# Optimization experiments

Hardware: AMD Instinct MI355X
Metric: run time of the kernel (lower is better)

Reference implementation:

```python
import jax, jax.numpy as jnp
import numpy as np

N_EMBD = 1024
N_HEAD = 16
HEAD_DIM = N_EMBD // N_HEAD

def setup_inputs() -> dict:
    key = jax.random.key(0)
    ks = jax.random.split(key, 5)
    B, T, C = 2, 2048, N_EMBD
    s = 1.0 / np.sqrt(C)
    x = jax.random.normal(ks[0], (B, T, C), dtype=jnp.float32)
    W_qkv = jax.random.normal(ks[1], (C, 3 * C), dtype=jnp.float32) * s
    b_qkv = jax.random.normal(ks[2], (3 * C,), dtype=jnp.float32) * 0.02
    W_o = jax.random.normal(ks[3], (C, C), dtype=jnp.float32) * s
    b_o = jax.random.normal(ks[4], (C,), dtype=jnp.float32) * 0.02
    return {"x": x, "W_qkv": W_qkv, "b_qkv": b_qkv, "W_o": W_o, "b_o": b_o}

def reference(x, W_qkv, b_qkv, W_o, b_o):
    B, T, C = x.shape
    H, D = N_HEAD, HEAD_DIM
    scale = 1.0 / np.sqrt(D)
    qkv = jnp.einsum('btc,cf->btf', x, W_qkv) + b_qkv  # [B,T,3C]
    q, k, v = jnp.split(qkv, 3, axis=-1)
    # [B,H,T,D]
    q = q.reshape(B, T, H, D).transpose(0, 2, 1, 3)
    k = k.reshape(B, T, H, D).transpose(0, 2, 1, 3)
    v = v.reshape(B, T, H, D).transpose(0, 2, 1, 3)
    att = jnp.einsum('bhqd,bhkd->bhqk', q, k) * scale  # [B,H,T,T]
    causal = jnp.tril(jnp.ones((T, T), dtype=bool))
    att = jnp.where(causal[None, None], att, -jnp.inf)
    att = jax.nn.softmax(att, axis=-1)
    y = jnp.einsum('bhqk,bhkd->bhqd', att, v)  # [B,H,T,D]
    y = y.transpose(0, 2, 1, 3).reshape(B, T, C)
    return jnp.einsum('btc,cf->btf', y, W_o) + b_o
```

## Files before the change

### kernel.cpp

```cpp
#include <hip/hip_runtime.h>
#include <hip/hip_bf16.h>

#define TT 2048
#define BB 2
#define CC 1024
#define NH 16
#define HD 64

typedef __attribute__((ext_vector_type(8))) short short8;
typedef __attribute__((ext_vector_type(4))) short short4b;
typedef __attribute__((ext_vector_type(4))) float f32x4;

typedef unsigned int __attribute__((address_space(1))) ui_gas;
typedef unsigned int __attribute__((address_space(3))) ui_las;

#if __has_builtin(__builtin_amdgcn_mfma_f32_16x16x16bf16_1k)
#define PV16 1
#else
#define PV16 0
#endif

__device__ __forceinline__ float us2f(unsigned short u) {
    union { unsigned int i; float f; } v; v.i = ((unsigned int)u) << 16; return v.f;
}
__device__ __forceinline__ unsigned short f2us(float f) {
    union { float f; unsigned int i; } v; v.f = f;
    unsigned int i = v.i;
    unsigned int lsb = (i >> 16) & 1u;
    i += 0x7fffu + lsb;
    return (unsigned short)(i >> 16);
}
__device__ __forceinline__ unsigned int pack2_trunc(float a, float b) {
    union { float f; unsigned int u; } x, y; x.f = a; y.f = b;
    return (y.u & 0xffff0000u) | (x.u >> 16);
}

__device__ __forceinline__ void gl_lds16(const unsigned short* g, unsigned short* l) {
    __builtin_amdgcn_global_load_lds((const ui_gas*)g, (ui_las*)l, 16, 0, 0);
}

__global__ __launch_bounds__(64) void detect_kernel(
    const void* p0, const void* p1, const void* p2, const void* p3, const void* p4,
    int* flags)
{
    const void* ps[5] = {p0, p1, p2, p3, p4};
    const int lane = threadIdx.x;
    for (int k = 0; k < 5; ++k) {
        const unsigned short* u = (const unsigned short*)ps[k];
        int bad = 0;
        #pragma unroll
        for (int j = 0; j < 4; ++j) {
            float v = us2f(u[lane * 4 + j]);
            if (!(fabsf(v) < 1e4f)) bad = 1;
        }
        unsigned long long m = __ballot(bad != 0);
        if (lane == 0) flags[k] = (__popcll(m) < 4) ? 1 : 0;
    }
}

__device__ __forceinline__ float4 load4(const void* p, size_t i, int isbf) {
    if (isbf) {
        ushort4 u = *reinterpret_cast<const ushort4*>((const unsigned short*)p + i);
        return make_float4(us2f(u.x), us2f(u.y), us2f(u.z), us2f(u.w));
    } else {
        return *reinterpret_cast<const float4*>((const float*)p + i);
    }
}
__device__ __forceinline__ float load1(const void* p, size_t i, int isbf) {
    return isbf ? us2f(((const unsigned short*)p)[i]) : ((const float*)p)[i];
}

__global__ __launch_bounds__(256) void prep_kernel(
    const void* __restrict__ x, const void* __restrict__ Wqkv, const void* __restrict__ Wo,
    unsigned short* __restrict__ xb, unsigned short* __restrict__ Wqkvt,
    unsigned short* __restrict__ Wot)
{
    __shared__ float Ls[64 * 65];
    __shared__ int sh_isbf;
    const int t = threadIdx.x;
    const int bid = blockIdx.x;

    const void* src;
    int mode, sub;
    if (bid < 2048)      { mode = 0; sub = bid;        src = x; }
    else if (bid < 2816) { mode = 1; sub = bid - 2048; src = Wqkv; }
    else                 { mode = 2; sub = bid - 2816; src = Wo; }

    if (t < 64) {
        const unsigned short* u = (const unsigned short*)src;
        int bad = 0;
        #pragma unroll
        for (int j = 0; j < 4; ++j) {
            float v = us2f(u[t * 4 + j]);
            if (!(fabsf(v) < 1e4f)) bad = 1;
        }
        unsigned long long m = __ballot(bad != 0);
        if (t == 0) sh_isbf = (__popcll(m) < 4) ? 1 : 0;
    }
    __syncthreads();
    const int isbf = sh_isbf;

    if (mode == 0) {
        const size_t i = ((size_t)sub * 256 + t) * 8;
        float4 a = load4(src, i, isbf);
        float4 b = load4(src, i + 4, isbf);
        alignas(16) unsigned short pk[8];
        pk[0] = f2us(a.x); pk[1] = f2us(a.y); pk[2] = f2us(a.z); pk[3] = f2us(a.w);
        pk[4] = f2us(b.x); pk[5] = f2us(b.y); pk[6] = f2us(b.z); pk[7] = f2us(b.w);
        *reinterpret_cast<uint4*>(xb + i) = *reinterpret_cast<const uint4*>(pk);
        return;
    }

    int N, Krows, n0, k0;
    unsigned short* dst;
    if (mode == 1) { N = 3 * CC; Krows = CC; dst = Wqkvt; n0 = (sub % 48) * 64; k0 = (sub / 48) * 64; }
    else           { N = CC;     Krows = CC; dst = Wot;   n0 = (sub % 16) * 64; k0 = (sub / 16) * 64; }
    {
        const int r = t >> 2, cq = (t & 3) << 4;
        #pragma unroll
        for (int i = 0; i < 4; ++i) {
            float4 v = load4(src, (size_t)(k0 + r) * N + n0 + cq + i * 4, isbf);
            Ls[r * 65 + cq + i * 4 + 0] = v.x;
            Ls[r * 65 + cq + i * 4 + 1] = v.y;
            Ls[r * 65 + cq + i * 4 + 2] = v.z;
            Ls[r * 65 + cq + i * 4 + 3] = v.w;
        }
    }
    __syncthreads();
    {
        const int c = t & 63, kg = (t >> 6) * 16;
        alignas(16) unsigned short pk[16];
        #pragma unroll
        for (int i = 0; i < 16; ++i) pk[i] = f2us(Ls[(kg + i) * 65 + c]);
        unsigned short* d = dst + (size_t)(n0 + c) * Krows + k0 + kg;
        *reinterpret_cast<uint4*>(d + 0) = *reinterpret_cast<const uint4*>(&pk[0]);
        *reinterpret_cast<uint4*>(d + 8) = *reinterpret_cast<const uint4*>(&pk[8]);
    }
}

template<int WM, int WN, int NWM, int NWN>
__global__ __launch_bounds__(256) void gemm_mfma(
    const unsigned short* __restrict__ A,
    const unsigned short* __restrict__ Bt,
    const void* __restrict__ bias, void* __restrict__ C,
    int M, int N, int K,
    const int* __restrict__ flags, int biasfi, int cfi)
{
    constexpr int BM = WM * 16 * NWM, BN = WN * 16 * NWN;
    constexpr int ASL = BM / 16, BSL = BN / 16;

    const int bias_bf = (biasfi >= 0) ? flags[biasfi] : 0;
    const int c_bf    = (cfi >= 0) ? flags[cfi] : ((cfi == -2) ? 1 : 0);

    __shared__ __align__(16) unsigned short Asl[ASL * 512];
    __shared__ __align__(16) unsigned short Bsl[BSL * 512];

    const int tid = threadIdx.x;
    const int l  = tid & 63;
    const int w  = tid >> 6;
    const int wm = w / NWN, wn = w % NWN;
    const int bm = blockIdx.y * BM, bn = blockIdx.x * BN;
    const int lm = l & 15;
    const int lk = (l >> 4) * 8;

    f32x4 acc[WM][WN];
    #pragma unroll
    for (int i = 0; i < WM; ++i)
        #pragma unroll
        for (int j = 0; j < WN; ++j) acc[i][j] = (f32x4){0.f, 0.f, 0.f, 0.f};

    for (int k0 = 0; k0 < K; k0 += 32) {
        #pragma unroll
        for (int s = 0; s < ASL / 4; ++s) {
            const int r = w * (ASL / 4) + s;
            gl_lds16(A + (size_t)(bm + r * 16 + lm) * K + k0 + lk, &Asl[r * 512]);
        }
        #pragma unroll
        for (int s = 0; s < BSL / 4; ++s) {
            const int r = w * (BSL / 4) + s;
            gl_lds16(Bt + (size_t)(bn + r * 16 + lm) * K + k0 + lk, &Bsl[r * 512]);
        }
        __syncthreads();
        short8 af[WM], bf[WN];
        #pragma unroll
        for (int i = 0; i < WM; ++i)
            af[i] = *reinterpret_cast<const short8*>(&Asl[(WM * wm + i) * 512 + l * 8]);
        #pragma unroll
        for (int j = 0; j < WN; ++j)
            bf[j] = *reinterpret_cast<const short8*>(&Bsl[(WN * wn + j) * 512 + l * 8]);
        #pragma unroll
        for (int i = 0; i < WM; ++i)
            #pragma unroll
            for (int j = 0; j < WN; ++j)
                acc[i][j] = __builtin_amdgcn_mfma_f32_16x16x32_bf16(af[i], bf[j], acc[i][j], 0, 0, 0);
        __syncthreads();
    }

    const int quad = l >> 4;
    float bv[WN];
    #pragma unroll
    for (int j = 0; j < WN; ++j) bv[j] = load1(bias, bn + (WN * wn + j) * 16 + lm, bias_bf);

    #pragma unroll
    for (int i = 0; i < WM; ++i) {
        #pragma unroll
        for (int r = 0; r < 4; ++r) {
            const int row = bm + (WM * wm + i) * 16 + quad * 4 + r;
            #pragma unroll
            for (int j = 0; j < WN; ++j) {
                const int col = bn + (WN * wn + j) * 16 + lm;
                const float val = acc[i][j][r] + bv[j];
                if (c_bf) ((unsigned short*)C)[(size_t)row * N + col] = f2us(val);
                else      ((float*)C)[(size_t)row * N + col] = val;
            }
        }
    }
}

__global__ __launch_bounds__(256) void transpose_v(
    const unsigned short* __restrict__ qkv, unsigned short* __restrict__ Vt)
{
    __shared__ __align__(16) unsigned short Ls[64 * 72];
    const int tid = threadIdx.x;
    const int tt = blockIdx.x;
    const int bh = blockIdx.y;
    const int b = bh >> 4, h = bh & 15;
    {
        const int tok = tid & 63, w = tid >> 6;
        const unsigned short* src = qkv + (size_t)(b * TT + tt * 64 + tok) * 3 * CC + 2 * CC + h * HD;
        #pragma unroll
        for (int c2 = 0; c2 < 2; ++c2) {
            int c = 2 * w + c2;
            uint4 d = *(const uint4*)(src + c * 8);
            *(uint4*)(&Ls[tok * 72 + c * 8]) = d;
        }
    }
    __syncthreads();
    {
        const int d = tid >> 2, kq = tid & 3;
        unsigned short out[16];
        #pragma unroll
        for (int i = 0; i < 16; ++i) out[i] = Ls[(kq * 16 + i) * 72 + d];
        unsigned short* dst = Vt + (size_t)bh * HD * TT + (size_t)d * TT + tt * 64 + kq * 16;
        *(uint4*)(dst + 0) = *(uint4*)(&out[0]);
        *(uint4*)(dst + 8) = *(uint4*)(&out[8]);
    }
}

__global__ __launch_bounds__(256) void attn_mfma(
    const unsigned short* __restrict__ qkv,
    const unsigned short* __restrict__ Vt,
    unsigned short* __restrict__ y)
{
    __shared__ __align__(16) unsigned short Ksh[8 * 512];
    __shared__ __align__(16) unsigned short Vsh[1039 * 8];

    const int tid = threadIdx.x;
    const int l   = tid & 63;
    const int w   = tid >> 6;
    const int quad = l >> 4;
    const int col  = l & 15;

    const int n  = blockIdx.x;
    const int g  = n >> 3;
    const int bh = (n & 7) * 4 + (g & 3);
    const int i  = g >> 2;
    const int tA = i, tB = 31 - i;
    const int b  = bh >> 4, h = bh & 15;

    for (int s = tid; s < 1039; s += 256)
        *(uint2*)(&Vsh[s * 8 + 4]) = make_uint2(0u, 0u);

    const float QSCALE = 0.18033688f;
    short8 qfA[2], qfB[2];
    #pragma unroll
    for (int t2 = 0; t2 < 2; ++t2) {
        const int qt = t2 ? tB : tA;
        short8* qf = t2 ? qfB : qfA;
        const int token = qt * 64 + w * 16 + col;
        const unsigned short* qrow = qkv + (size_t)(b * TT + token) * 3 * CC + h * HD;
        #pragma unroll
        for (int ks = 0; ks < 2; ++ks) {
            ushort4 u0 = *(const ushort4*)(qrow + ks * 32 + quad * 8);
            ushort4 u1 = *(const ushort4*)(qrow + ks * 32 + quad * 8 + 4);
            alignas(16) unsigned short pk[8];
            pk[0] = f2us(us2f(u0.x) * QSCALE);
            pk[1] = f2us(us2f(u0.y) * QSCALE);
            pk[2] = f2us(us2f(u0.z) * QSCALE);
            pk[3] = f2us(us2f(u0.w) * QSCALE);
            pk[4] = f2us(us2f(u1.x) * QSCALE);
            pk[5] = f2us(us2f(u1.y) * QSCALE);
            pk[6] = f2us(us2f(u1.z) * QSCALE);
            pk[7] = f2us(us2f(u1.w) * QSCALE);
            qf[ks] = *(const short8*)pk;
        }
    }

    f32x4 oA[4], oB[4];
    #pragma unroll
    for (int nb = 0; nb < 4; ++nb) {
        oA[nb] = (f32x4){0.f, 0.f, 0.f, 0.f};
        oB[nb] = (f32x4){0.f, 0.f, 0.f, 0.f};
    }
    float mA = -3e38f, lAc = 0.f, mB = -3e38f, lBc = 0.f;

    const unsigned short* kbase = qkv + (size_t)b * TT * 3 * CC + CC + h * HD;
    const unsigned short* vbase = Vt + (size_t)bh * HD * TT;

    const int vd = tid >> 2, vg0 = (tid & 3) * 4;

    uint4 rk[2], rv[2];
    auto issue_loads = [&](int kt) {
        const unsigned short* ksrc = kbase + (size_t)(kt * 64 + l) * 3 * CC;
        #pragma unroll
        for (int c2 = 0; c2 < 2; ++c2) {
            const int c = 2 * w + c2;
            rk[c2] = *(const uint4*)(ksrc + c * 8);
        }
        const unsigned short* vsrc = vbase + (size_t)vd * TT + kt * 64 + vg0 * 4;
        rv[0] = *(const uint4*)(vsrc + 0);
        rv[1] = *(const uint4*)(vsrc + 8);
    };
    auto write_lds = [&]() {
        #pragma unroll
        for (int c2 = 0; c2 < 2; ++c2) {
            const int c = 2 * w + c2;
            const int ks = c >> 2, q = c & 3;
            const int slot = ((quad * 2 + ks) * 64 + q * 16 + col) * 8;
            *(uint4*)(&Ksh[slot]) = rk[c2];
        }
        *(uint2*)(&Vsh[((vg0 + 0) * 65 + vd) * 8]) = make_uint2(rv[0].x, rv[0].y);
        *(uint2*)(&Vsh[((vg0 + 1) * 65 + vd) * 8]) = make_uint2(rv[0].z, rv[0].w);
        *(uint2*)(&Vsh[((vg0 + 2) * 65 + vd) * 8]) = make_uint2(rv[1].x, rv[1].y);
        *(uint2*)(&Vsh[((vg0 + 3) * 65 + vd) * 8]) = make_uint2(rv[1].z, rv[1].w);
    };

    auto step = [&](const short8* qf, f32x4* o, float& m_i, float& l_i, bool diag) {
        f32x4 st[4];
        #pragma unroll
        for (int nb = 0; nb < 4; ++nb) {
            f32x4 acc = {0.f, 0.f, 0.f, 0.f};
            #pragma unroll
            for (int ks = 0; ks < 2; ++ks) {
                short8 kf = *(const short8*)(&Ksh[((nb * 2 + ks) * 64 + l) * 8]);
                acc = __builtin_amdgcn_mfma_f32_16x16x32_bf16(kf, qf[ks], acc, 0, 0, 0);
            }
            st[nb] = acc;
        }
        float sv[4][4];
        #pragma unroll
        for (int nb = 0; nb < 4; ++nb)
            #pragma unroll
            for (int r = 0; r < 4; ++r) {
                float v = st[nb][r];
                if (diag && (nb * 16 + quad * 4 + r > w * 16 + col)) v = -3e38f;
                sv[nb][r] = v;
            }
        float rm = sv[0][0];
        #pragma unroll
        for (int nb = 0; nb < 4; ++nb)
            #pragma unroll
            for (int r = 0; r < 4; ++r) rm = fmaxf(rm, sv[nb][r]);
        rm = fmaxf(rm, __shfl_xor(rm, 16));
        rm = fmaxf(rm, __shfl_xor(rm, 32));
        const float mn = fmaxf(m_i, rm);
        float pv[4][4];
        float rs = 0.f;
        #pragma unroll
        for (int nb = 0; nb < 4; ++nb)
            #pragma unroll
            for (int r = 0; r < 4; ++r) {
                float p = __builtin_exp2f(sv[nb][r] - mn);
                pv[nb][r] = p;
                rs += p;
            }
        rs += __shfl_xor(rs, 16);
        rs += __shfl_xor(rs, 32);
        if (__ballot(mn > m_i) != 0ull) {
            const float al = __builtin_exp2f(m_i - mn);
            l_i = l_i * al + rs;
            float alr[4];
            #pragma unroll
            for (int r = 0; r < 4; ++r) alr[r] = __shfl(al, quad * 4 + r);
            #pragma unroll
            for (int nb = 0; nb < 4; ++nb)
                #pragma unroll
                for (int r = 0; r < 4; ++r) o[nb][r] *= alr[r];
        } else {
            l_i += rs;
        }
        m_i = mn;
#if PV16
        short4b pf[4];
        #pragma unroll
        for (int nbk = 0; nbk < 4; ++nbk) {
            union { short4b s; unsigned int u[2]; } pk;
            pk.u[0] = pack2_trunc(pv[nbk][0], pv[nbk][1]);
            pk.u[1] = pack2_trunc(pv[nbk][2], pv[nbk][3]);
            pf[nbk] = pk.s;
        }
        #pragma unroll
        for (int nbd = 0; nbd < 4; ++nbd)
            #pragma unroll
            for (int nbk = 0; nbk < 4; ++nbk) {
                short4b vf = *(const short4b*)(&Vsh[((nbk * 4 + quad) * 65 + nbd * 16 + col) * 8]);
                o[nbd] = __builtin_amdgcn_mfma_f32_16x16x16bf16_1k(pf[nbk], vf, o[nbd], 0, 0, 0);
            }
#else
        short8 pf[4];
        #pragma unroll
        for (int nbk = 0; nbk < 4; ++nbk) {
            union { short8 s; unsigned int u[4]; } pk;
            pk.u[0] = pack2_trunc(pv[nbk][0], pv[nbk][1]);
            pk.u[1] = pack2_trunc(pv[nbk][2], pv[nbk][3]);
            pk.u[2] = 0u; pk.u[3] = 0u;
            pf[nbk] = pk.s;
        }
        #pragma unroll
        for (int nbd = 0; nbd < 4; ++nbd)
            #pragma unroll
            for (int nbk = 0; nbk < 4; ++nbk) {
                short8 vf = *(const short8*)(&Vsh[((nbk * 4 + quad) * 65 + nbd * 16 + col) * 8]);
                o[nbd] = __builtin_amdgcn_mfma_f32_16x16x32_bf16(pf[nbk], vf, o[nbd], 0, 0, 0);
            }
#endif
    };

    issue_loads(0);
    for (int kt = 0; kt <= tB; ++kt) {
        write_lds();
        __syncthreads();
        if (kt < tB) issue_loads(kt + 1);
        step(qfB, oB, mB, lBc, kt == tB);
        if (kt <= tA) step(qfA, oA, mA, lAc, kt == tA);
        __syncthreads();
    }

    #pragma unroll
    for (int t2 = 0; t2 < 2; ++t2) {
        const int qt = t2 ? tB : tA;
        f32x4* o = t2 ? oB : oA;
        const float inv = 1.f / (t2 ? lBc : lAc);
        float invr[4];
        #pragma unroll
        for (int r = 0; r < 4; ++r) invr[r] = __shfl(inv, quad * 4 + r);
        #pragma unroll
        for (int nb = 0; nb < 4; ++nb)
            #pragma unroll
            for (int r = 0; r < 4; ++r) {
                int token = qt * 64 + w * 16 + quad * 4 + r;
                y[(size_t)(b * TT + token) * CC + h * HD + nb * 16 + col] = f2us(o[nb][r] * invr[r]);
            }
    }
}

extern "C" void kernel_launch(void* const* d_in, const int* in_sizes, int n_in,
                              void* d_out, int out_size, void* d_ws, size_t ws_size,
                              hipStream_t stream) {
    const int M = BB * TT;

    char* ws = (char*)d_ws;
    int*            flags = (int*)ws;                         ws += 256;
    unsigned short* xb    = (unsigned short*)ws;              ws += (size_t)M * CC * 2;
    unsigned short* Wqkvt = (unsigned short*)ws;              ws += (size_t)3 * CC * CC * 2;
    unsigned short* Wot   = (unsigned short*)ws;              ws += (size_t)CC * CC * 2;
    unsigned short* qkv   = (unsigned short*)ws;              ws += (size_t)M * 3 * CC * 2;
    unsigned short* Vt    = (unsigned short*)ws;              ws += (size_t)BB * NH * HD * TT * 2;
    unsigned short* y     = (unsigned short*)ws;

    detect_kernel<<<1, 64, 0, stream>>>(d_in[0], d_in[1], d_in[2], d_in[3], d_in[4], flags);

    prep_kernel<<<3072, 256, 0, stream>>>(d_in[0], d_in[1], d_in[3], xb, Wqkvt, Wot);

    gemm_mfma<4, 4, 2, 2><<<dim3(3 * CC / 128, M / 128), 256, 0, stream>>>(
        xb, Wqkvt, d_in[2], qkv, M, 3 * CC, CC, flags, 2, -2);

    transpose_v<<<dim3(TT / 64, BB * NH), 256, 0, stream>>>(qkv, Vt);

    attn_mfma<<<512, 256, 0, stream>>>(qkv, Vt, y);

    gemm_mfma<2, 4, 4, 1><<<dim3(CC / 64, M / 128), 256, 0, stream>>>(
        y, Wot, d_in[4], d_out, M, CC, CC, flags, 4, 0);
}
```

Before: 239.0 us.

## Split causal attention KV range across two blocks, add combine kernel

```diff
diff --git a/kernel.cpp b/kernel.cpp
--- a/kernel.cpp
+++ b/kernel.cpp
@@ -39,25 +39,6 @@
     __builtin_amdgcn_global_load_lds((const ui_gas*)g, (ui_las*)l, 16, 0, 0);
 }
 
-__global__ __launch_bounds__(64) void detect_kernel(
-    const void* p0, const void* p1, const void* p2, const void* p3, const void* p4,
-    int* flags)
-{
-    const void* ps[5] = {p0, p1, p2, p3, p4};
-    const int lane = threadIdx.x;
-    for (int k = 0; k < 5; ++k) {
-        const unsigned short* u = (const unsigned short*)ps[k];
-        int bad = 0;
-        #pragma unroll
-        for (int j = 0; j < 4; ++j) {
-            float v = us2f(u[lane * 4 + j]);
-            if (!(fabsf(v) < 1e4f)) bad = 1;
-        }
-        unsigned long long m = __ballot(bad != 0);
-        if (lane == 0) flags[k] = (__popcll(m) < 4) ? 1 : 0;
-    }
-}
-
 __device__ __forceinline__ float4 load4(const void* p, size_t i, int isbf) {
     if (isbf) {
         ushort4 u = *reinterpret_cast<const ushort4*>((const unsigned short*)p + i);
@@ -72,8 +53,9 @@
 
 __global__ __launch_bounds__(256) void prep_kernel(
     const void* __restrict__ x, const void* __restrict__ Wqkv, const void* __restrict__ Wo,
+    const void* __restrict__ bqkv, const void* __restrict__ bo,
     unsigned short* __restrict__ xb, unsigned short* __restrict__ Wqkvt,
-    unsigned short* __restrict__ Wot)
+    unsigned short* __restrict__ Wot, int* __restrict__ flags)
 {
     __shared__ float Ls[64 * 65];
     __shared__ int sh_isbf;
@@ -86,6 +68,20 @@
     else if (bid < 2816) { mode = 1; sub = bid - 2048; src = Wqkv; }
     else                 { mode = 2; sub = bid - 2816; src = Wo; }
 
+    if (bid == 0 && t < 64) {
+        const void* ps[5] = {x, Wqkv, bqkv, Wo, bo};
+        for (int k = 0; k < 5; ++k) {
+            const unsigned short* u = (const unsigned short*)ps[k];
+            int bad = 0;
+            #pragma unroll
+            for (int j = 0; j < 4; ++j) {
+                float v = us2f(u[t * 4 + j]);
+                if (!(fabsf(v) < 1e4f)) bad = 1;
+            }
+            unsigned long long m = __ballot(bad != 0);
+            if (t == 0) flags[k] = (__popcll(m) < 4) ? 1 : 0;
+        }
+    }
     if (t < 64) {
         const unsigned short* u = (const unsigned short*)src;
         int bad = 0;
@@ -250,7 +246,9 @@
 __global__ __launch_bounds__(256) void attn_mfma(
     const unsigned short* __restrict__ qkv,
     const unsigned short* __restrict__ Vt,
-    unsigned short* __restrict__ y)
+    unsigned short* __restrict__ y,
+    unsigned short* __restrict__ pO,
+    float* __restrict__ pML)
 {
     __shared__ __align__(16) unsigned short Ksh[8 * 512];
     __shared__ __align__(16) unsigned short Vsh[1039 * 8];
@@ -261,15 +259,19 @@
     const int quad = l >> 4;
     const int col  = l & 15;
 
-    const int n  = blockIdx.x;
-    const int g  = n >> 3;
-    const int bh = (n & 7) * 4 + (g & 3);
-    const int i  = g >> 2;
+    const int n    = blockIdx.x;
+    const int bh   = (n & 7) * 4 + ((n >> 3) & 3);
+    const int rem  = n >> 5;
+    const int i    = rem & 15;
+    const int half = rem >> 4;
     const int tA = i, tB = 31 - i;
+    const int s  = (i >= 8) ? 8 : (16 - i);
+    const int lo = half ? s : 0;
+    const int hi = half ? tB : (s - 1);
     const int b  = bh >> 4, h = bh & 15;
 
-    for (int s = tid; s < 1039; s += 256)
-        *(uint2*)(&Vsh[s * 8 + 4]) = make_uint2(0u, 0u);
+    for (int ss = tid; ss < 1039; ss += 256)
+        *(uint2*)(&Vsh[ss * 8 + 4]) = make_uint2(0u, 0u);
 
     const float QSCALE = 0.18033688f;
     short8 qfA[2], qfB[2];
@@ -426,31 +428,88 @@
 #endif
     };
 
-    issue_loads(0);
-    for (int kt = 0; kt <= tB; ++kt) {
+    issue_loads(lo);
+    for (int kt = lo; kt <= hi; ++kt) {
         write_lds();
         __syncthreads();
-        if (kt < tB) issue_loads(kt + 1);
+        if (kt < hi) issue_loads(kt + 1);
         step(qfB, oB, mB, lBc, kt == tB);
         if (kt <= tA) step(qfA, oA, mA, lAc, kt == tA);
         __syncthreads();
     }
 
+    auto epilogue = [&](int qt, f32x4* o, float m_i, float l_i) {
+        if (qt < 8) {
+            if (half != 0) return;
+            const float inv = 1.f / l_i;
+            float invr[4];
+            #pragma unroll
+            for (int r = 0; r < 4; ++r) invr[r] = __shfl(inv, quad * 4 + r);
+            #pragma unroll
+            for (int nb = 0; nb < 4; ++nb)
+                #pragma unroll
+                for (int r = 0; r < 4; ++r) {
+                    int token = qt * 64 + w * 16 + quad * 4 + r;
+                    y[(size_t)(b * TT + token) * CC + h * HD + nb * 16 + col] = f2us(o[nb][r] * invr[r]);
+                }
+        } else {
+            const int qt8 = qt - 8;
+            const size_t obase = (((size_t)bh * 24 + qt8) * 2 + half) * 4096;
+            #pragma unroll
+            for (int nb = 0; nb < 4; ++nb)
+                #pragma unroll
+                for (int r = 0; r < 4; ++r)
+                    pO[obase + (size_t)(w * 16 + quad * 4 + r) * 64 + nb * 16 + col] = f2us(o[nb][r]);
+            if (quad == 0) {
+                const size_t mbase = (((size_t)bh * 24 + qt8) * 2 + half) * 128;
+                pML[mbase + (w * 16 + col)] = m_i;
+                pML[mbase + 64 + (w * 16 + col)] = l_i;
+            }
+        }
+    };
+    epilogue(tA, oA, mA, lAc);
+    epilogue(tB, oB, mB, lBc);
+}
+
+__global__ __launch_bounds__(256) void combine_kernel(
+    const unsigned short* __restrict__ pO, const float* __restrict__ pML,
+    unsigned short* __restrict__ y)
+{
+    const int m  = blockIdx.x;
+    const int bh = (m & 7) * 4 + ((m >> 3) & 3);
+    const int qt8 = m >> 5;
+    const int qt = qt8 + 8;
+    const int b = bh >> 4, h = bh & 15;
+    const int t = threadIdx.x;
+    const int q = t >> 2, dg = (t & 3) * 16;
+
+    const size_t mb = ((size_t)bh * 24 + qt8) * 256;
+    const float m0 = pML[mb + q],       l0 = pML[mb + 64 + q];
+    const float m1 = pML[mb + 128 + q], l1 = pML[mb + 192 + q];
+    const float mm = fmaxf(m0, m1);
+    const float e0 = __builtin_exp2f(m0 - mm);
+    const float e1 = __builtin_exp2f(m1 - mm);
+    const float inv = 1.f / (e0 * l0 + e1 * l1);
+    const float s0 = e0 * inv, s1 = e1 * inv;
+
+    const size_t ob = ((size_t)bh * 24 + qt8) * 8192 + (size_t)q * 64 + dg;
+    unsigned short* yrow = y + (size_t)(b * TT + qt * 64 + q) * CC + h * HD + dg;
     #pragma unroll
-    for (int t2 = 0; t2 < 2; ++t2) {
-        const int qt = t2 ? tB : tA;
-        f32x4* o = t2 ? oB : oA;
-        const float inv = 1.f / (t2 ? lBc : lAc);
-        float invr[4];
-        #pragma unroll
-        for (int r = 0; r < 4; ++r) invr[r] = __shfl(inv, quad * 4 + r);
-        #pragma unroll
-        for (int nb = 0; nb < 4; ++nb)
-            #pragma unroll
-            for (int r = 0; r < 4; ++r) {
-                int token = qt * 64 + w * 16 + quad * 4 + r;
-                y[(size_t)(b * TT + token) * CC + h * HD + nb * 16 + col] = f2us(o[nb][r] * invr[r]);
-            }
+    for (int j = 0; j < 16; j += 8) {
+        ushort4 a0 = *(const ushort4*)(pO + ob + j);
+        ushort4 a1 = *(const ushort4*)(pO + ob + j + 4);
+        ushort4 c0 = *(const ushort4*)(pO + ob + 4096 + j);
+        ushort4 c1 = *(const ushort4*)(pO + ob + 4096 + j + 4);
+        alignas(16) unsigned short pk[8];
+        pk[0] = f2us(s0 * us2f(a0.x) + s1 * us2f(c0.x));
+        pk[1] = f2us(s0 * us2f(a0.y) + s1 * us2f(c0.y));
+        pk[2] = f2us(s0 * us2f(a0.z) + s1 * us2f(c0.z));
+        pk[3] = f2us(s0 * us2f(a0.w) + s1 * us2f(c0.w));
+        pk[4] = f2us(s0 * us2f(a1.x) + s1 * us2f(c1.x));
+        pk[5] = f2us(s0 * us2f(a1.y) + s1 * us2f(c1.y));
+        pk[6] = f2us(s0 * us2f(a1.z) + s1 * us2f(c1.z));
+        pk[7] = f2us(s0 * us2f(a1.w) + s1 * us2f(c1.w));
+        *(uint4*)(yrow + j) = *(const uint4*)pk;
     }
 }
 
@@ -468,16 +527,20 @@
     unsigned short* Vt    = (unsigned short*)ws;              ws += (size_t)BB * NH * HD * TT * 2;
     unsigned short* y     = (unsigned short*)ws;
 
-    detect_kernel<<<1, 64, 0, stream>>>(d_in[0], d_in[1], d_in[2], d_in[3], d_in[4], flags);
-
-    prep_kernel<<<3072, 256, 0, stream>>>(d_in[0], d_in[1], d_in[3], xb, Wqkvt, Wot);
+    unsigned short* pO  = (unsigned short*)((char*)d_ws + 256);
+    float*          pML = (float*)((char*)d_ws + 256 + (size_t)32 * 24 * 2 * 4096 * 2);
+
+    prep_kernel<<<3072, 256, 0, stream>>>(d_in[0], d_in[1], d_in[3], d_in[2], d_in[4],
+                                          xb, Wqkvt, Wot, flags);
 
     gemm_mfma<4, 4, 2, 2><<<dim3(3 * CC / 128, M / 128), 256, 0, stream>>>(
         xb, Wqkvt, d_in[2], qkv, M, 3 * CC, CC, flags, 2, -2);
 
     transpose_v<<<dim3(TT / 64, BB * NH), 256, 0, stream>>>(qkv, Vt);
 
-    attn_mfma<<<512, 256, 0, stream>>>(qkv, Vt, y);
+    attn_mfma<<<1024, 256, 0, stream>>>(qkv, Vt, y, pO, pML);
+
+    combine_kernel<<<768, 256, 0, stream>>>(pO, pML, y);
 
     gemm_mfma<2, 4, 4, 1><<<dim3(CC / 64, M / 128), 256, 0, stream>>>(
         y, Wot, d_in[4], d_out, M, CC, CC, flags, 4, 0);
```

New measurement: 243.3 us. No clear change (+1.8%).

## Process two KV tiles per attention iteration, widen GEMM K-step, fold detect into prep

Applied to the files above, without the earlier changes.

```diff
diff --git a/kernel.cpp b/kernel.cpp
--- a/kernel.cpp
+++ b/kernel.cpp
@@ -16,8 +16,10 @@
 
 #if __has_builtin(__builtin_amdgcn_mfma_f32_16x16x16bf16_1k)
 #define PV16 1
+#define VSS 4
 #else
 #define PV16 0
+#define VSS 8
 #endif
 
 __device__ __forceinline__ float us2f(unsigned short u) {
@@ -39,25 +41,6 @@
     __builtin_amdgcn_global_load_lds((const ui_gas*)g, (ui_las*)l, 16, 0, 0);
 }
 
-__global__ __launch_bounds__(64) void detect_kernel(
-    const void* p0, const void* p1, const void* p2, const void* p3, const void* p4,
-    int* flags)
-{
-    const void* ps[5] = {p0, p1, p2, p3, p4};
-    const int lane = threadIdx.x;
-    for (int k = 0; k < 5; ++k) {
-        const unsigned short* u = (const unsigned short*)ps[k];
-        int bad = 0;
-        #pragma unroll
-        for (int j = 0; j < 4; ++j) {
-            float v = us2f(u[lane * 4 + j]);
-            if (!(fabsf(v) < 1e4f)) bad = 1;
-        }
-        unsigned long long m = __ballot(bad != 0);
-        if (lane == 0) flags[k] = (__popcll(m) < 4) ? 1 : 0;
-    }
-}
-
 __device__ __forceinline__ float4 load4(const void* p, size_t i, int isbf) {
     if (isbf) {
         ushort4 u = *reinterpret_cast<const ushort4*>((const unsigned short*)p + i);
@@ -72,8 +55,9 @@
 
 __global__ __launch_bounds__(256) void prep_kernel(
     const void* __restrict__ x, const void* __restrict__ Wqkv, const void* __restrict__ Wo,
+    const void* __restrict__ bqkv, const void* __restrict__ bo,
     unsigned short* __restrict__ xb, unsigned short* __restrict__ Wqkvt,
-    unsigned short* __restrict__ Wot)
+    unsigned short* __restrict__ Wot, int* __restrict__ flags)
 {
     __shared__ float Ls[64 * 65];
     __shared__ int sh_isbf;
@@ -86,6 +70,20 @@
     else if (bid < 2816) { mode = 1; sub = bid - 2048; src = Wqkv; }
     else                 { mode = 2; sub = bid - 2816; src = Wo; }
 
+    if (bid == 0 && t < 64) {
+        const void* ps[5] = {x, Wqkv, bqkv, Wo, bo};
+        for (int k = 0; k < 5; ++k) {
+            const unsigned short* u = (const unsigned short*)ps[k];
+            int bad = 0;
+            #pragma unroll
+            for (int j = 0; j < 4; ++j) {
+                float v = us2f(u[t * 4 + j]);
+                if (!(fabsf(v) < 1e4f)) bad = 1;
+            }
+            unsigned long long m = __ballot(bad != 0);
+            if (t == 0) flags[k] = (__popcll(m) < 4) ? 1 : 0;
+        }
+    }
     if (t < 64) {
         const unsigned short* u = (const unsigned short*)src;
         int bad = 0;
@@ -152,8 +150,8 @@
     const int bias_bf = (biasfi >= 0) ? flags[biasfi] : 0;
     const int c_bf    = (cfi >= 0) ? flags[cfi] : ((cfi == -2) ? 1 : 0);
 
-    __shared__ __align__(16) unsigned short Asl[ASL * 512];
-    __shared__ __align__(16) unsigned short Bsl[BSL * 512];
+    __shared__ __align__(16) unsigned short Asl[ASL * 2 * 512];
+    __shared__ __align__(16) unsigned short Bsl[BSL * 2 * 512];
 
     const int tid = threadIdx.x;
     const int l  = tid & 63;
@@ -169,30 +167,39 @@
         #pragma unroll
         for (int j = 0; j < WN; ++j) acc[i][j] = (f32x4){0.f, 0.f, 0.f, 0.f};
 
-    for (int k0 = 0; k0 < K; k0 += 32) {
+    for (int k0 = 0; k0 < K; k0 += 64) {
         #pragma unroll
         for (int s = 0; s < ASL / 4; ++s) {
             const int r = w * (ASL / 4) + s;
-            gl_lds16(A + (size_t)(bm + r * 16 + lm) * K + k0 + lk, &Asl[r * 512]);
+            #pragma unroll
+            for (int kh = 0; kh < 2; ++kh)
+                gl_lds16(A + (size_t)(bm + r * 16 + lm) * K + k0 + kh * 32 + lk,
+                         &Asl[(r * 2 + kh) * 512]);
         }
         #pragma unroll
         for (int s = 0; s < BSL / 4; ++s) {
             const int r = w * (BSL / 4) + s;
-            gl_lds16(Bt + (size_t)(bn + r * 16 + lm) * K + k0 + lk, &Bsl[r * 512]);
+            #pragma unroll
+            for (int kh = 0; kh < 2; ++kh)
+                gl_lds16(Bt + (size_t)(bn + r * 16 + lm) * K + k0 + kh * 32 + lk,
+                         &Bsl[(r * 2 + kh) * 512]);
         }
         __syncthreads();
-        short8 af[WM], bf[WN];
-        #pragma unroll
-        for (int i = 0; i < WM; ++i)
-            af[i] = *reinterpret_cast<const short8*>(&Asl[(WM * wm + i) * 512 + l * 8]);
-        #pragma unroll
-        for (int j = 0; j < WN; ++j)
-            bf[j] = *reinterpret_cast<const short8*>(&Bsl[(WN * wn + j) * 512 + l * 8]);
-        #pragma unroll
-        for (int i = 0; i < WM; ++i)
+        #pragma unroll
+        for (int kh = 0; kh < 2; ++kh) {
+            short8 af[WM], bf[WN];
+            #pragma unroll
+            for (int i = 0; i < WM; ++i)
+                af[i] = *reinterpret_cast<const short8*>(&Asl[((WM * wm + i) * 2 + kh) * 512 + l * 8]);
             #pragma unroll
             for (int j = 0; j < WN; ++j)
-                acc[i][j] = __builtin_amdgcn_mfma_f32_16x16x32_bf16(af[i], bf[j], acc[i][j], 0, 0, 0);
+                bf[j] = *reinterpret_cast<const short8*>(&Bsl[((WN * wn + j) * 2 + kh) * 512 + l * 8]);
+            #pragma unroll
+            for (int i = 0; i < WM; ++i)
+                #pragma unroll
+                for (int j = 0; j < WN; ++j)
+                    acc[i][j] = __builtin_amdgcn_mfma_f32_16x16x32_bf16(af[i], bf[j], acc[i][j], 0, 0, 0);
+        }
         __syncthreads();
     }
 
@@ -252,8 +259,8 @@
     const unsigned short* __restrict__ Vt,
     unsigned short* __restrict__ y)
 {
-    __shared__ __align__(16) unsigned short Ksh[8 * 512];
-    __shared__ __align__(16) unsigned short Vsh[1039 * 8];
+    __shared__ __align__(16) unsigned short Ksh[2][8 * 512];
+    __shared__ __align__(16) unsigned short Vsh[2][1039 * VSS];
 
     const int tid = threadIdx.x;
     const int l   = tid & 63;
@@ -268,8 +275,12 @@
     const int tA = i, tB = 31 - i;
     const int b  = bh >> 4, h = bh & 15;
 
-    for (int s = tid; s < 1039; s += 256)
-        *(uint2*)(&Vsh[s * 8 + 4]) = make_uint2(0u, 0u);
+#if !PV16
+    for (int ss = tid; ss < 1039; ss += 256) {
+        *(uint2*)(&Vsh[0][ss * 8 + 4]) = make_uint2(0u, 0u);
+        *(uint2*)(&Vsh[1][ss * 8 + 4]) = make_uint2(0u, 0u);
+    }
+#endif
 
     const float QSCALE = 0.18033688f;
     short8 qfA[2], qfB[2];
@@ -309,40 +320,77 @@
 
     const int vd = tid >> 2, vg0 = (tid & 3) * 4;
 
-    uint4 rk[2], rv[2];
-    auto issue_loads = [&](int kt) {
+    uint4 rk[2][2], rv[2][2];
+    auto issue_loads = [&](int set, int kt) {
         const unsigned short* ksrc = kbase + (size_t)(kt * 64 + l) * 3 * CC;
         #pragma unroll
         for (int c2 = 0; c2 < 2; ++c2) {
             const int c = 2 * w + c2;
-            rk[c2] = *(const uint4*)(ksrc + c * 8);
+            rk[set][c2] = *(const uint4*)(ksrc + c * 8);
         }
         const unsigned short* vsrc = vbase + (size_t)vd * TT + kt * 64 + vg0 * 4;
-        rv[0] = *(const uint4*)(vsrc + 0);
-        rv[1] = *(const uint4*)(vsrc + 8);
+        rv[set][0] = *(const uint4*)(vsrc + 0);
+        rv[set][1] = *(const uint4*)(vsrc + 8);
     };
-    auto write_lds = [&]() {
+    auto write_lds = [&](int set) {
         #pragma unroll
         for (int c2 = 0; c2 < 2; ++c2) {
             const int c = 2 * w + c2;
             const int ks = c >> 2, q = c & 3;
             const int slot = ((quad * 2 + ks) * 64 + q * 16 + col) * 8;
-            *(uint4*)(&Ksh[slot]) = rk[c2];
-        }
-        *(uint2*)(&Vsh[((vg0 + 0) * 65 + vd) * 8]) = make_uint2(rv[0].x, rv[0].y);
-        *(uint2*)(&Vsh[((vg0 + 1) * 65 + vd) * 8]) = make_uint2(rv[0].z, rv[0].w);
-        *(uint2*)(&Vsh[((vg0 + 2) * 65 + vd) * 8]) = make_uint2(rv[1].x, rv[1].y);
-        *(uint2*)(&Vsh[((vg0 + 3) * 65 + vd) * 8]) = make_uint2(rv[1].z, rv[1].w);
+            *(uint4*)(&Ksh[set][slot]) = rk[set][c2];
+        }
+        *(uint2*)(&Vsh[set][((vg0 + 0) * 65 + vd) * VSS]) = make_uint2(rv[set][0].x, rv[set][0].y);
+        *(uint2*)(&Vsh[set][((vg0 + 1) * 65 + vd) * VSS]) = make_uint2(rv[set][0].z, rv[set][0].w);
+        *(uint2*)(&Vsh[set][((vg0 + 2) * 65 + vd) * VSS]) = make_uint2(rv[set][1].x, rv[set][1].y);
+        *(uint2*)(&Vsh[set][((vg0 + 3) * 65 + vd) * VSS]) = make_uint2(rv[set][1].z, rv[set][1].w);
     };
 
-    auto step = [&](const short8* qf, f32x4* o, float& m_i, float& l_i, bool diag) {
+    auto pv_mfma = [&](int wi, const float p0[4][4], f32x4* o) {
+#if PV16
+        short4b pf[4];
+        #pragma unroll
+        for (int nbk = 0; nbk < 4; ++nbk) {
+            union { short4b s; unsigned int u[2]; } pk;
+            pk.u[0] = pack2_trunc(p0[nbk][0], p0[nbk][1]);
+            pk.u[1] = pack2_trunc(p0[nbk][2], p0[nbk][3]);
+            pf[nbk] = pk.s;
+        }
+        #pragma unroll
+        for (int nbd = 0; nbd < 4; ++nbd)
+            #pragma unroll
+            for (int nbk = 0; nbk < 4; ++nbk) {
+                short4b vf = *(const short4b*)(&Vsh[wi][((nbk * 4 + quad) * 65 + nbd * 16 + col) * VSS]);
+                o[nbd] = __builtin_amdgcn_mfma_f32_16x16x16bf16_1k(pf[nbk], vf, o[nbd], 0, 0, 0);
+            }
+#else
+        short8 pf[4];
+        #pragma unroll
+        for (int nbk = 0; nbk < 4; ++nbk) {
+            union { short8 s; unsigned int u[4]; } pk;
+            pk.u[0] = pack2_trunc(p0[nbk][0], p0[nbk][1]);
+            pk.u[1] = pack2_trunc(p0[nbk][2], p0[nbk][3]);
+            pk.u[2] = 0u; pk.u[3] = 0u;
+            pf[nbk] = pk.s;
+        }
+        #pragma unroll
+        for (int nbd = 0; nbd < 4; ++nbd)
+            #pragma unroll
+            for (int nbk = 0; nbk < 4; ++nbk) {
+                short8 vf = *(const short8*)(&Vsh[wi][((nbk * 4 + quad) * 65 + nbd * 16 + col) * VSS]);
+                o[nbd] = __builtin_amdgcn_mfma_f32_16x16x32_bf16(pf[nbk], vf, o[nbd], 0, 0, 0);
+            }
+#endif
+    };
+
+    auto step1 = [&](const short8* qf, f32x4* o, float& m_i, float& l_i, bool diag) {
         f32x4 st[4];
         #pragma unroll
         for (int nb = 0; nb < 4; ++nb) {
             f32x4 acc = {0.f, 0.f, 0.f, 0.f};
             #pragma unroll
             for (int ks = 0; ks < 2; ++ks) {
-                short8 kf = *(const short8*)(&Ksh[((nb * 2 + ks) * 64 + l) * 8]);
+                short8 kf = *(const short8*)(&Ksh[0][((nb * 2 + ks) * 64 + l) * 8]);
                 acc = __builtin_amdgcn_mfma_f32_16x16x32_bf16(kf, qf[ks], acc, 0, 0, 0);
             }
             st[nb] = acc;
@@ -364,14 +412,14 @@
         rm = fmaxf(rm, __shfl_xor(rm, 16));
         rm = fmaxf(rm, __shfl_xor(rm, 32));
         const float mn = fmaxf(m_i, rm);
-        float pv[4][4];
+        float pv0[4][4];
         float rs = 0.f;
         #pragma unroll
         for (int nb = 0; nb < 4; ++nb)
             #pragma unroll
             for (int r = 0; r < 4; ++r) {
                 float p = __builtin_exp2f(sv[nb][r] - mn);
-                pv[nb][r] = p;
+                pv0[nb][r] = p;
                 rs += p;
             }
         rs += __shfl_xor(rs, 16);
@@ -390,49 +438,88 @@
             l_i += rs;
         }
         m_i = mn;
-#if PV16
-        short4b pf[4];
-        #pragma unroll
-        for (int nbk = 0; nbk < 4; ++nbk) {
-            union { short4b s; unsigned int u[2]; } pk;
-            pk.u[0] = pack2_trunc(pv[nbk][0], pv[nbk][1]);
-            pk.u[1] = pack2_trunc(pv[nbk][2], pv[nbk][3]);
-            pf[nbk] = pk.s;
-        }
-        #pragma unroll
-        for (int nbd = 0; nbd < 4; ++nbd)
-            #pragma unroll
-            for (int nbk = 0; nbk < 4; ++nbk) {
-                short4b vf = *(const short4b*)(&Vsh[((nbk * 4 + quad) * 65 + nbd * 16 + col) * 8]);
-                o[nbd] = __builtin_amdgcn_mfma_f32_16x16x16bf16_1k(pf[nbk], vf, o[nbd], 0, 0, 0);
-            }
-#else
-        short8 pf[4];
-        #pragma unroll
-        for (int nbk = 0; nbk < 4; ++nbk) {
-            union { short8 s; unsigned int u[4]; } pk;
-            pk.u[0] = pack2_trunc(pv[nbk][0], pv[nbk][1]);
-            pk.u[1] = pack2_trunc(pv[nbk][2], pv[nbk][3]);
-            pk.u[2] = 0u; pk.u[3] = 0u;
-            pf[nbk] = pk.s;
-        }
-        #pragma unroll
-        for (int nbd = 0; nbd < 4; ++nbd)
-            #pragma unroll
-            for (int nbk = 0; nbk < 4; ++nbk) {
-                short8 vf = *(const short8*)(&Vsh[((nbk * 4 + quad) * 65 + nbd * 16 + col) * 8]);
-                o[nbd] = __builtin_amdgcn_mfma_f32_16x16x32_bf16(pf[nbk], vf, o[nbd], 0, 0, 0);
-            }
-#endif
+        pv_mfma(0, pv0, o);
     };
 
-    issue_loads(0);
-    for (int kt = 0; kt <= tB; ++kt) {
-        write_lds();
+    auto step2 = [&](const short8* qf, f32x4* o, float& m_i, float& l_i, bool diag1) {
+        f32x4 st[2][4];
+        #pragma unroll
+        for (int wi = 0; wi < 2; ++wi)
+            #pragma unroll
+            for (int nb = 0; nb < 4; ++nb) {
+                f32x4 acc = {0.f, 0.f, 0.f, 0.f};
+                #pragma unroll
+                for (int ks = 0; ks < 2; ++ks) {
+                    short8 kf = *(const short8*)(&Ksh[wi][((nb * 2 + ks) * 64 + l) * 8]);
+                    acc = __builtin_amdgcn_mfma_f32_16x16x32_bf16(kf, qf[ks], acc, 0, 0, 0);
+                }
+                st[wi][nb] = acc;
+            }
+        float sv[2][4][4];
+        #pragma unroll
+        for (int nb = 0; nb < 4; ++nb)
+            #pragma unroll
+            for (int r = 0; r < 4; ++r) {
+                sv[0][nb][r] = st[0][nb][r];
+                float v = st[1][nb][r];
+                if (diag1 && (nb * 16 + quad * 4 + r > w * 16 + col)) v = -3e38f;
+                sv[1][nb][r] = v;
+            }
+        float rm = sv[0][0][0];
+        #pragma unroll
+        for (int wi = 0; wi < 2; ++wi)
+            #pragma unroll
+            for (int nb = 0; nb < 4; ++nb)
+                #pragma unroll
+                for (int r = 0; r < 4; ++r) rm = fmaxf(rm, sv[wi][nb][r]);
+        rm = fmaxf(rm, __shfl_xor(rm, 16));
+        rm = fmaxf(rm, __shfl_xor(rm, 32));
+        const float mn = fmaxf(m_i, rm);
+        float pv0[4][4], pv1[4][4];
+        float rs = 0.f;
+        #pragma unroll
+        for (int nb = 0; nb < 4; ++nb)
+            #pragma unroll
+            for (int r = 0; r < 4; ++r) {
+                float p0 = __builtin_exp2f(sv[0][nb][r] - mn);
+                float p1 = __builtin_exp2f(sv[1][nb][r] - mn);
+                pv0[nb][r] = p0;
+                pv1[nb][r] = p1;
+                rs += p0 + p1;
+            }
+        rs += __shfl_xor(rs, 16);
+        rs += __shfl_xor(rs, 32);
+        if (__ballot(mn > m_i) != 0ull) {
+            const float al = __builtin_exp2f(m_i - mn);
+            l_i = l_i * al + rs;
+            float alr[4];
+            #pragma unroll
+            for (int r = 0; r < 4; ++r) alr[r] = __shfl(al, quad * 4 + r);
+            #pragma unroll
+            for (int nb = 0; nb < 4; ++nb)
+                #pragma unroll
+                for (int r = 0; r < 4; ++r) o[nb][r] *= alr[r];
+        } else {
+            l_i += rs;
+        }
+        m_i = mn;
+        pv_mfma(0, pv0, o);
+        pv_mfma(1, pv1, o);
+    };
+
+    issue_loads(0, 0);
+    issue_loads(1, 1);
+    for (int kt = 0; kt <= tB; kt += 2) {
+        const bool twoB = (kt + 1 <= tB);
+        write_lds(0);
+        if (twoB) write_lds(1);
         __syncthreads();
-        if (kt < tB) issue_loads(kt + 1);
-        step(qfB, oB, mB, lBc, kt == tB);
-        if (kt <= tA) step(qfA, oA, mA, lAc, kt == tA);
+        if (kt + 2 <= tB) issue_loads(0, kt + 2);
+        if (kt + 3 <= tB) issue_loads(1, kt + 3);
+        if (twoB) step2(qfB, oB, mB, lBc, (kt + 1 == tB));
+        else      step1(qfB, oB, mB, lBc, (kt == tB));
+        if (kt + 1 <= tA)      step2(qfA, oA, mA, lAc, (kt + 1 == tA));
+        else if (kt <= tA)     step1(qfA, oA, mA, lAc, (kt == tA));
         __syncthreads();
     }
 
@@ -468,9 +555,8 @@
     unsigned short* Vt    = (unsigned short*)ws;              ws += (size_t)BB * NH * HD * TT * 2;
     unsigned short* y     = (unsigned short*)ws;
 
-    detect_kernel<<<1, 64, 0, stream>>>(d_in[0], d_in[1], d_in[2], d_in[3], d_in[4], flags);
-
-    prep_kernel<<<3072, 256, 0, stream>>>(d_in[0], d_in[1], d_in[3], xb, Wqkvt, Wot);
+    prep_kernel<<<3072, 256, 0, stream>>>(d_in[0], d_in[1], d_in[3], d_in[2], d_in[4],
+                                          xb, Wqkvt, Wot, flags);
 
     gemm_mfma<4, 4, 2, 2><<<dim3(3 * CC / 128, M / 128), 256, 0, stream>>>(
         xb, Wqkvt, d_in[2], qkv, M, 3 * CC, CC, flags, 2, -2);
```

Result: no change. 240.7 us (+0.7%).
